# Kernel tuning notes

Hardware: AMD Instinct MI355X
Metric: run time of the kernel (lower is better)

The kernel has to match this reference:

```python
import jax, jax.numpy as jnp
import numpy as np

HEAD_SIZE = 64


def setup_inputs() -> dict:
    key = jax.random.key(0)
    kx, kk, kq, kv = jax.random.split(key, 4)
    B, T, C = 4, 4096, 1024
    x = jax.random.normal(kx, (B, T, C), dtype=jnp.float32)
    Wk = jax.random.normal(kk, (C, HEAD_SIZE), dtype=jnp.float32) * 0.02
    Wq = jax.random.normal(kq, (C, HEAD_SIZE), dtype=jnp.float32) * 0.02
    Wv = jax.random.normal(kv, (C, HEAD_SIZE), dtype=jnp.float32) * 0.02
    return {"x": x, "Wk": Wk, "Wq": Wq, "Wv": Wv}


def reference(x, Wk, Wq, Wv):
    # x: (B,T,C); projections to (B,T,H)
    T = x.shape[1]
    k = jnp.einsum('btc,ch->bth', x, Wk)
    q = jnp.einsum('btc,ch->bth', x, Wq)
    v = jnp.einsum('btc,ch->bth', x, Wv)
    scale = 1.0 / jnp.sqrt(jnp.float32(HEAD_SIZE))
    wei = jnp.einsum('bth,bsh->bts', q, k) * scale  # (B,T,T)
    causal = jnp.tril(jnp.ones((T, T), dtype=bool))
    wei = jnp.where(causal, wei, -jnp.inf)
    wei = jax.nn.softmax(wei, axis=-1)
    out = jnp.einsum('bts,bsh->bth', wei, v)  # (B,T,H)
    return out
```

## Files before the change

### kernel.cpp

```cpp
#include <hip/hip_runtime.h>

typedef __attribute__((ext_vector_type(8))) short short8;
typedef __attribute__((ext_vector_type(4))) float f32x4;
typedef unsigned short u16;

#define BB 4
#define TT 4096
#define CC 1024
#define HH 64

static __device__ __forceinline__ u16 f2bf(float f) {
    unsigned int u = __float_as_uint(f);
    unsigned int r = (u + 0x7FFFu + ((u >> 16) & 1u)) >> 16;
    return (u16)r;
}

static __device__ __forceinline__ int swz(int row, int chunk) {
    return row * 64 + ((chunk ^ (row & 7)) << 3);
}

__global__ void detect_dtype(const u16* __restrict__ xu, int* __restrict__ flag) {
    int lane = threadIdx.x;
    int cnt = 0;
    for (int i = lane; i < 1024; i += 64) {
        u16 u = xu[2 * i];
        int e = (u >> 7) & 0xFF;
        cnt += (e >= 100 && e <= 140) ? 1 : 0;
    }
    for (int d = 1; d < 64; d <<= 1) cnt += __shfl_xor(cnt, d);
    if (lane == 0) *flag = (cnt > 512) ? 1 : 0;
}

__global__ void wt_transpose(const void* __restrict__ Wk, const void* __restrict__ Wq,
                             const void* __restrict__ Wv, u16* __restrict__ Wtp,
                             float* __restrict__ accz, const int* __restrict__ flag) {
    if (blockIdx.x >= 192) {
        int zb = blockIdx.x - 192;
        const int n4 = (BB * TT * HH + BB * TT) / 4;
        float4 z = {0.f, 0.f, 0.f, 0.f};
        for (int i = zb * 256 + threadIdx.x; i < n4; i += 256 * 256)
            reinterpret_cast<float4*>(accz)[i] = z;
        return;
    }
    const int isbf = *flag;
    int r = blockIdx.x;
    int p = r >> 6;
    int n = r & 63;
    int nt = n >> 4, nl = n & 15;
    const void* W = (p == 0) ? Wq : (p == 1) ? Wk : Wv;
    int k0 = threadIdx.x * 4;
    int kb = k0 >> 6, k2 = (k0 >> 5) & 1, quad = (k0 >> 3) & 3, half = (k0 >> 2) & 1;
    ushort4 v;
    if (isbf) {
        const u16* Wb = (const u16*)W;
        v.x = Wb[(k0 + 0) * HH + n]; v.y = Wb[(k0 + 1) * HH + n];
        v.z = Wb[(k0 + 2) * HH + n]; v.w = Wb[(k0 + 3) * HH + n];
    } else {
        const float* Wf = (const float*)W;
        v.x = f2bf(Wf[(k0 + 0) * HH + n]); v.y = f2bf(Wf[(k0 + 1) * HH + n]);
        v.z = f2bf(Wf[(k0 + 2) * HH + n]); v.w = f2bf(Wf[(k0 + 3) * HH + n]);
    }
    size_t off16 = ((size_t)((p * 4 + nt) * 16 + kb) * 2 + k2) * 64 + quad * 16 + nl;
    *reinterpret_cast<ushort4*>(Wtp + off16 * 8 + half * 4) = v;
}

__global__ __launch_bounds__(256) void qkv_proj(const void* __restrict__ x,
                                                const u16* __restrict__ Wtp,
                                                u16* __restrict__ qo, u16* __restrict__ ko,
                                                u16* __restrict__ vo, const int* __restrict__ flag) {
    __shared__ __align__(16) u16 xs[16 * 1024];
    __shared__ __align__(16) u16 tls[4][3][256];
    const int isbf = *flag;
    const int tid = threadIdx.x;
    const int lane = tid & 63;
    const int w = tid >> 6;
    const int l15 = lane & 15;
    const int quad = lane >> 4;
    int phys = blockIdx.x;
    int rb = (phys & 7) * 128 + (phys >> 3);
    const int g0r = rb * 16;

    #pragma unroll
    for (int j = 0; j < 8; j++) {
        int c = tid + j * 256;
        int row = c >> 7, ck = c & 127;
        int dst = row * 1024 + ((ck ^ (row & 7)) << 3);
        if (isbf) {
            uint4 d = *reinterpret_cast<const uint4*>((const u16*)x + (size_t)(g0r + row) * CC + ck * 8);
            *reinterpret_cast<uint4*>(xs + dst) = d;
        } else {
            const float4* pf = reinterpret_cast<const float4*>((const float*)x + (size_t)(g0r + row) * CC + ck * 8);
            float4 a0 = pf[0], a1 = pf[1];
            ushort4 lo; lo.x = f2bf(a0.x); lo.y = f2bf(a0.y); lo.z = f2bf(a0.z); lo.w = f2bf(a0.w);
            ushort4 hi; hi.x = f2bf(a1.x); hi.y = f2bf(a1.y); hi.z = f2bf(a1.z); hi.w = f2bf(a1.w);
            *reinterpret_cast<ushort4*>(xs + dst) = lo;
            *reinterpret_cast<ushort4*>(xs + dst + 4) = hi;
        }
    }
    __syncthreads();

    f32x4 zero = {0.f, 0.f, 0.f, 0.f};
    f32x4 acc[3];
    #pragma unroll
    for (int i = 0; i < 3; i++) acc[i] = zero;

    for (int kb = 0; kb < 16; kb++) {
        #pragma unroll
        for (int k2 = 0; k2 < 2; k2++) {
            int ck = kb * 8 + k2 * 4 + quad;
            short8 af = *reinterpret_cast<const short8*>(xs + l15 * 1024 + ((ck ^ (l15 & 7)) << 3));
            #pragma unroll
            for (int p = 0; p < 3; p++) {
                short8 bf = *reinterpret_cast<const short8*>(
                    Wtp + ((((size_t)(p * 4 + w) * 16 + kb) * 2 + k2) * 64 + lane) * 8);
                acc[p] = __builtin_amdgcn_mfma_f32_16x16x32_bf16(af, bf, acc[p], 0, 0, 0);
            }
        }
    }

    const float qscale = 0.18033688011112042f;
    #pragma unroll
    for (int p = 0; p < 3; p++) {
        if (p < 2) {
            float sc = (p == 0) ? qscale : 1.f;
            #pragma unroll
            for (int r = 0; r < 4; r++)
                tls[w][p][(quad * 4 + r) * 16 + l15] = f2bf(acc[p][r] * sc);
        } else {
            #pragma unroll
            for (int r = 0; r < 4; r++)
                tls[w][p][l15 * 16 + quad * 4 + r] = f2bf(acc[p][r]);
        }
    }
    #pragma unroll
    for (int p = 0; p < 2; p++) {
        int t = lane >> 2, seg = lane & 3;
        ushort4 d = *reinterpret_cast<const ushort4*>(&tls[w][p][t * 16 + seg * 4]);
        u16* dst = (p == 0) ? qo : ko;
        *reinterpret_cast<ushort4*>(dst + (size_t)(g0r + t) * HH + w * 16 + seg * 4) = d;
    }
    {
        int c = lane >> 2, seg = lane & 3;
        ushort4 d = *reinterpret_cast<const ushort4*>(&tls[w][2][c * 16 + seg * 4]);
        int b = rb >> 8;
        int kt = (g0r & 4095) >> 6;
        int toff = g0r & 63;
        *reinterpret_cast<ushort4*>(vo + ((size_t)((b * 64 + kt) * 64 + w * 16 + c)) * 64 + toff + seg * 4) = d;
    }
}

__global__ __launch_bounds__(256) void attn(const u16* __restrict__ qp, const u16* __restrict__ kp,
                                            const u16* __restrict__ vp, float* __restrict__ acco,
                                            float* __restrict__ accl, void* __restrict__ outv,
                                            const int* __restrict__ flag, int nsplit) {
    __shared__ __align__(16) u16 kst[64 * 64];
    __shared__ __align__(16) u16 vts[64 * 64];
    __shared__ __align__(16) u16 pb[4][16 * 64];
    const int isbf = *flag;
    const int tid = threadIdx.x;
    const int lane = tid & 63;
    const int w = tid >> 6;
    const int l15 = lane & 15;
    const int quad = lane >> 4;

    int u = blockIdx.x;
    int b, qt, ks;
    if (nsplit == 1) {
        b = u >> 6;
        int raw = u & 63;
        qt = (raw & 1) ? (63 - (raw >> 1)) : (raw >> 1);
        ks = 0;
    } else {
        int per = 64 * nsplit;
        b = u / per;
        int rem = u - b * per;
        qt = rem / nsplit;
        ks = rem - qt * nsplit;
    }
    int qbase = qt * 64;
    int diag = qt;
    int nkt = diag + 1;
    if (ks >= nkt) return;

    short8 aq[2];
    {
        const u16* qrow = qp + (size_t)(b * TT + qbase + w * 16 + l15) * HH;
        aq[0] = *reinterpret_cast<const short8*>(qrow + quad * 8);
        aq[1] = *reinterpret_cast<const short8*>(qrow + 32 + quad * 8);
    }

    f32x4 zero = {0.f, 0.f, 0.f, 0.f};
    f32x4 o[4];
    #pragma unroll
    for (int i = 0; i < 4; i++) o[i] = zero;
    f32x4 lsum = zero;

    for (int kt = ks; kt < nkt; kt += nsplit) {
        __syncthreads();
        #pragma unroll
        for (int j = 0; j < 2; j++) {
            int cc = tid + j * 256;
            int row = cc >> 3, c8 = cc & 7;
            int dst = swz(row, c8);
            uint4 dk = *reinterpret_cast<const uint4*>(kp + (size_t)(b * TT + kt * 64) * HH + cc * 8);
            *reinterpret_cast<uint4*>(&kst[dst]) = dk;
            uint4 dv = *reinterpret_cast<const uint4*>(vp + ((size_t)(b * 64 + kt)) * 64 * 64 + cc * 8);
            *reinterpret_cast<uint4*>(&vts[dst]) = dv;
        }
        __syncthreads();
        f32x4 s[4];
        #pragma unroll
        for (int i = 0; i < 4; i++) s[i] = zero;
        #pragma unroll
        for (int k2 = 0; k2 < 2; k2++) {
            #pragma unroll
            for (int nt = 0; nt < 4; nt++) {
                short8 bf = *reinterpret_cast<const short8*>(&kst[swz(nt * 16 + l15, k2 * 4 + quad)]);
                s[nt] = __builtin_amdgcn_mfma_f32_16x16x32_bf16(aq[k2], bf, s[nt], 0, 0, 0);
            }
        }
        const int rg = qbase + w * 16 + quad * 4;
        const bool dm = (kt == diag);
        #pragma unroll
        for (int nt = 0; nt < 4; nt++) {
            int key = kt * 64 + nt * 16 + l15;
            #pragma unroll
            for (int r = 0; r < 4; r++) {
                float p = __builtin_amdgcn_exp2f(s[nt][r]);
                if (dm && key > rg + r) p = 0.f;
                s[nt][r] = p;
            }
        }
        #pragma unroll
        for (int nt = 0; nt < 4; nt++) lsum = lsum + s[nt];
        #pragma unroll
        for (int nt = 0; nt < 4; nt++) {
            int chunk = nt * 2 + (l15 >> 3);
            int off = l15 & 7;
            #pragma unroll
            for (int r = 0; r < 4; r++) {
                int row = quad * 4 + r;
                pb[w][row * 64 + ((chunk ^ (row & 7)) << 3) + off] = f2bf(s[nt][r]);
            }
        }
        #pragma unroll
        for (int k2 = 0; k2 < 2; k2++) {
            short8 ap = *reinterpret_cast<const short8*>(&pb[w][swz(l15, k2 * 4 + quad)]);
            #pragma unroll
            for (int nt = 0; nt < 4; nt++) {
                short8 bv = *reinterpret_cast<const short8*>(&vts[swz(nt * 16 + l15, k2 * 4 + quad)]);
                o[nt] = __builtin_amdgcn_mfma_f32_16x16x32_bf16(ap, bv, o[nt], 0, 0, 0);
            }
        }
    }

    #pragma unroll
    for (int d = 1; d < 16; d <<= 1) {
        f32x4 t;
        #pragma unroll
        for (int r = 0; r < 4; r++) t[r] = __shfl_xor(lsum[r], d);
        lsum = lsum + t;
    }
    const int g0 = b * TT + qbase + w * 16 + quad * 4;

    if (nsplit == 1) {
        f32x4 inv;
        #pragma unroll
        for (int r = 0; r < 4; r++) inv[r] = 1.0f / lsum[r];
        if (isbf) {
            u16* outp = (u16*)outv;
            #pragma unroll
            for (int nt = 0; nt < 4; nt++)
                #pragma unroll
                for (int r = 0; r < 4; r++)
                    outp[(size_t)(g0 + r) * HH + nt * 16 + l15] = f2bf(o[nt][r] * inv[r]);
        } else {
            float* outp = (float*)outv;
            #pragma unroll
            for (int nt = 0; nt < 4; nt++)
                #pragma unroll
                for (int r = 0; r < 4; r++)
                    outp[(size_t)(g0 + r) * HH + nt * 16 + l15] = o[nt][r] * inv[r];
        }
    } else {
        #pragma unroll
        for (int nt = 0; nt < 4; nt++)
            #pragma unroll
            for (int r = 0; r < 4; r++)
                atomicAdd(&acco[(size_t)(g0 + r) * HH + nt * 16 + l15], o[nt][r]);
        if (l15 == 0) {
            #pragma unroll
            for (int r = 0; r < 4; r++) atomicAdd(&accl[g0 + r], lsum[r]);
        }
    }
}

__global__ __launch_bounds__(256) void attn_finalize(const float* __restrict__ acco,
                                                     const float* __restrict__ accl,
                                                     void* __restrict__ outv,
                                                     const int* __restrict__ flag) {
    const int isbf = *flag;
    int i = blockIdx.x * blockDim.x + threadIdx.x;
    int row = i >> 4;
    float4 ov = reinterpret_cast<const float4*>(acco)[i];
    float inv = 1.0f / accl[row];
    if (isbf) {
        ushort4 s;
        s.x = f2bf(ov.x * inv); s.y = f2bf(ov.y * inv);
        s.z = f2bf(ov.z * inv); s.w = f2bf(ov.w * inv);
        reinterpret_cast<ushort4*>(outv)[i] = s;
    } else {
        float4 s = {ov.x * inv, ov.y * inv, ov.z * inv, ov.w * inv};
        reinterpret_cast<float4*>(outv)[i] = s;
    }
}

extern "C" void kernel_launch(void* const* d_in, const int* in_sizes, int n_in,
                              void* d_out, int out_size, void* d_ws, size_t ws_size,
                              hipStream_t stream) {
    const void* x  = d_in[0];
    const void* Wk = d_in[1];
    const void* Wq = d_in[2];
    const void* Wv = d_in[3];
    char* ws = (char*)d_ws;
    u16* qo = (u16*)(ws);
    u16* ko = (u16*)(ws + (size_t)2 * 1024 * 1024);
    u16* vo = (u16*)(ws + (size_t)4 * 1024 * 1024);
    u16* Wtp = (u16*)(ws + (size_t)6 * 1024 * 1024);
    int* flag = (int*)(ws + (size_t)6 * 1024 * 1024 + 768 * 1024);
    float* acco = (float*)(ws + (size_t)7 * 1024 * 1024);
    float* accl = (float*)(ws + (size_t)11 * 1024 * 1024);

    const size_t need_split = (size_t)11 * 1024 * 1024 + 128 * 1024;
    const int nsplit = (ws_size >= need_split) ? 4 : 1;

    detect_dtype<<<1, 64, 0, stream>>>((const u16*)x, flag);
    wt_transpose<<<(nsplit > 1 ? 448 : 192), 256, 0, stream>>>(Wk, Wq, Wv, Wtp, acco, flag);
    qkv_proj<<<1024, 256, 0, stream>>>(x, Wtp, qo, ko, vo, flag);
    if (nsplit > 1) {
        attn<<<BB * 64 * nsplit, 256, 0, stream>>>(qo, ko, vo, acco, accl, d_out, flag, nsplit);
        attn_finalize<<<(BB * TT * HH / 4) / 256, 256, 0, stream>>>(acco, accl, d_out, flag);
    } else {
        attn<<<BB * 64, 256, 0, stream>>>(qo, ko, vo, acco, accl, d_out, flag, 1);
    }
}
```

Baseline: 154.7 us.

## Drop dtype-detect kernel, prefetch K/V tiles, replace split atomics with partial buffers

Removes the separate dtype-detection launch by having each kernel probe the input with a wavefront ballot. It also drops the accumulator zeroing that used to live in the transpose launch. The attention loop now prefetches the next K/V tile into registers while the current one is committed to LDS, with lighter barriers. Split-K partial results go to per-split buffers instead of atomics, and the finalize kernel sums them. This cuts launch count, atomic contention and load latency, at the cost of a larger workspace and repeated probe loads in every block.

```diff
diff --git a/kernel.cpp b/kernel.cpp
--- a/kernel.cpp
+++ b/kernel.cpp
@@ -15,34 +15,27 @@
     return (u16)r;
 }
 
+static __device__ __forceinline__ int probe_isbf(const u16* xu) {
+    int lane = threadIdx.x & 63;
+    u16 u = xu[lane * 32];
+    int e = (u >> 7) & 0xFF;
+    unsigned long long m = __ballot(e >= 100 && e <= 140);
+    return __popcll(m) > 32;
+}
+
+static __device__ __forceinline__ void bar_lds() {
+    __builtin_amdgcn_s_waitcnt(0xC07F);
+    __builtin_amdgcn_s_barrier();
+}
+
 static __device__ __forceinline__ int swz(int row, int chunk) {
     return row * 64 + ((chunk ^ (row & 7)) << 3);
 }
 
-__global__ void detect_dtype(const u16* __restrict__ xu, int* __restrict__ flag) {
-    int lane = threadIdx.x;
-    int cnt = 0;
-    for (int i = lane; i < 1024; i += 64) {
-        u16 u = xu[2 * i];
-        int e = (u >> 7) & 0xFF;
-        cnt += (e >= 100 && e <= 140) ? 1 : 0;
-    }
-    for (int d = 1; d < 64; d <<= 1) cnt += __shfl_xor(cnt, d);
-    if (lane == 0) *flag = (cnt > 512) ? 1 : 0;
-}
-
 __global__ void wt_transpose(const void* __restrict__ Wk, const void* __restrict__ Wq,
                              const void* __restrict__ Wv, u16* __restrict__ Wtp,
-                             float* __restrict__ accz, const int* __restrict__ flag) {
-    if (blockIdx.x >= 192) {
-        int zb = blockIdx.x - 192;
-        const int n4 = (BB * TT * HH + BB * TT) / 4;
-        float4 z = {0.f, 0.f, 0.f, 0.f};
-        for (int i = zb * 256 + threadIdx.x; i < n4; i += 256 * 256)
-            reinterpret_cast<float4*>(accz)[i] = z;
-        return;
-    }
-    const int isbf = *flag;
+                             const u16* __restrict__ xprobe) {
+    const int isbf = probe_isbf(xprobe);
     int r = blockIdx.x;
     int p = r >> 6;
     int n = r & 63;
@@ -67,10 +60,10 @@
 __global__ __launch_bounds__(256) void qkv_proj(const void* __restrict__ x,
                                                 const u16* __restrict__ Wtp,
                                                 u16* __restrict__ qo, u16* __restrict__ ko,
-                                                u16* __restrict__ vo, const int* __restrict__ flag) {
+                                                u16* __restrict__ vo) {
     __shared__ __align__(16) u16 xs[16 * 1024];
     __shared__ __align__(16) u16 tls[4][3][256];
-    const int isbf = *flag;
+    const int isbf = probe_isbf((const u16*)x);
     const int tid = threadIdx.x;
     const int lane = tid & 63;
     const int w = tid >> 6;
@@ -150,13 +143,13 @@
 }
 
 __global__ __launch_bounds__(256) void attn(const u16* __restrict__ qp, const u16* __restrict__ kp,
-                                            const u16* __restrict__ vp, float* __restrict__ acco,
+                                            const u16* __restrict__ vp, float* __restrict__ accp,
                                             float* __restrict__ accl, void* __restrict__ outv,
-                                            const int* __restrict__ flag, int nsplit) {
+                                            const u16* __restrict__ xprobe, int nsplit) {
     __shared__ __align__(16) u16 kst[64 * 64];
     __shared__ __align__(16) u16 vts[64 * 64];
     __shared__ __align__(16) u16 pb[4][16 * 64];
-    const int isbf = *flag;
+    const int isbf = probe_isbf(xprobe);
     const int tid = threadIdx.x;
     const int lane = tid & 63;
     const int w = tid >> 6;
@@ -195,19 +188,32 @@
     for (int i = 0; i < 4; i++) o[i] = zero;
     f32x4 lsum = zero;
 
-    for (int kt = ks; kt < nkt; kt += nsplit) {
-        __syncthreads();
+    uint4 pk[2], pv[2];
+    auto pref = [&](int kt2) {
+        #pragma unroll
+        for (int j = 0; j < 2; j++) {
+            int cc = tid + j * 256;
+            pk[j] = *reinterpret_cast<const uint4*>(kp + (size_t)(b * TT + kt2 * 64) * HH + cc * 8);
+            pv[j] = *reinterpret_cast<const uint4*>(vp + ((size_t)(b * 64 + kt2)) * 64 * 64 + cc * 8);
+        }
+    };
+    auto commit = [&]() {
         #pragma unroll
         for (int j = 0; j < 2; j++) {
             int cc = tid + j * 256;
             int row = cc >> 3, c8 = cc & 7;
             int dst = swz(row, c8);
-            uint4 dk = *reinterpret_cast<const uint4*>(kp + (size_t)(b * TT + kt * 64) * HH + cc * 8);
-            *reinterpret_cast<uint4*>(&kst[dst]) = dk;
-            uint4 dv = *reinterpret_cast<const uint4*>(vp + ((size_t)(b * 64 + kt)) * 64 * 64 + cc * 8);
-            *reinterpret_cast<uint4*>(&vts[dst]) = dv;
-        }
-        __syncthreads();
+            *reinterpret_cast<uint4*>(&kst[dst]) = pk[j];
+            *reinterpret_cast<uint4*>(&vts[dst]) = pv[j];
+        }
+    };
+
+    pref(ks);
+    for (int kt = ks; kt < nkt; kt += nsplit) {
+        bar_lds();
+        commit();
+        if (kt + nsplit < nkt) pref(kt + nsplit);
+        bar_lds();
         f32x4 s[4];
         #pragma unroll
         for (int i = 0; i < 4; i++) s[i] = zero;
@@ -283,34 +289,43 @@
                     outp[(size_t)(g0 + r) * HH + nt * 16 + l15] = o[nt][r] * inv[r];
         }
     } else {
+        float* op = accp + (size_t)ks * TT * BB * HH;
         #pragma unroll
         for (int nt = 0; nt < 4; nt++)
             #pragma unroll
             for (int r = 0; r < 4; r++)
-                atomicAdd(&acco[(size_t)(g0 + r) * HH + nt * 16 + l15], o[nt][r]);
+                op[(size_t)(g0 + r) * HH + nt * 16 + l15] = o[nt][r];
         if (l15 == 0) {
             #pragma unroll
-            for (int r = 0; r < 4; r++) atomicAdd(&accl[g0 + r], lsum[r]);
-        }
-    }
-}
-
-__global__ __launch_bounds__(256) void attn_finalize(const float* __restrict__ acco,
+            for (int r = 0; r < 4; r++) accl[ks * (TT * BB) + g0 + r] = lsum[r];
+        }
+    }
+}
+
+__global__ __launch_bounds__(256) void attn_finalize(const float* __restrict__ accp,
                                                      const float* __restrict__ accl,
                                                      void* __restrict__ outv,
-                                                     const int* __restrict__ flag) {
-    const int isbf = *flag;
+                                                     const u16* __restrict__ xprobe, int nsplit) {
+    const int isbf = probe_isbf(xprobe);
     int i = blockIdx.x * blockDim.x + threadIdx.x;
     int row = i >> 4;
-    float4 ov = reinterpret_cast<const float4*>(acco)[i];
-    float inv = 1.0f / accl[row];
+    int qt = (row & (TT - 1)) >> 6;
+    int nv = min(nsplit, qt + 1);
+    float4 o = {0.f, 0.f, 0.f, 0.f};
+    float l = 0.f;
+    for (int ks = 0; ks < nv; ks++) {
+        float4 t = reinterpret_cast<const float4*>(accp + (size_t)ks * TT * BB * HH)[i];
+        o.x += t.x; o.y += t.y; o.z += t.z; o.w += t.w;
+        l += accl[ks * (TT * BB) + row];
+    }
+    float inv = 1.0f / l;
     if (isbf) {
         ushort4 s;
-        s.x = f2bf(ov.x * inv); s.y = f2bf(ov.y * inv);
-        s.z = f2bf(ov.z * inv); s.w = f2bf(ov.w * inv);
+        s.x = f2bf(o.x * inv); s.y = f2bf(o.y * inv);
+        s.z = f2bf(o.z * inv); s.w = f2bf(o.w * inv);
         reinterpret_cast<ushort4*>(outv)[i] = s;
     } else {
-        float4 s = {ov.x * inv, ov.y * inv, ov.z * inv, ov.w * inv};
+        float4 s = {o.x * inv, o.y * inv, o.z * inv, o.w * inv};
         reinterpret_cast<float4*>(outv)[i] = s;
     }
 }
@@ -327,20 +342,16 @@
     u16* ko = (u16*)(ws + (size_t)2 * 1024 * 1024);
     u16* vo = (u16*)(ws + (size_t)4 * 1024 * 1024);
     u16* Wtp = (u16*)(ws + (size_t)6 * 1024 * 1024);
-    int* flag = (int*)(ws + (size_t)6 * 1024 * 1024 + 768 * 1024);
-    float* acco = (float*)(ws + (size_t)7 * 1024 * 1024);
-    float* accl = (float*)(ws + (size_t)11 * 1024 * 1024);
-
-    const size_t need_split = (size_t)11 * 1024 * 1024 + 128 * 1024;
+    float* accp = (float*)(ws + (size_t)7 * 1024 * 1024);
+    float* accl = (float*)(ws + (size_t)23 * 1024 * 1024);
+
+    const size_t need_split = (size_t)23 * 1024 * 1024 + 512 * 1024;
     const int nsplit = (ws_size >= need_split) ? 4 : 1;
-
-    detect_dtype<<<1, 64, 0, stream>>>((const u16*)x, flag);
-    wt_transpose<<<(nsplit > 1 ? 448 : 192), 256, 0, stream>>>(Wk, Wq, Wv, Wtp, acco, flag);
-    qkv_proj<<<1024, 256, 0, stream>>>(x, Wtp, qo, ko, vo, flag);
-    if (nsplit > 1) {
-        attn<<<BB * 64 * nsplit, 256, 0, stream>>>(qo, ko, vo, acco, accl, d_out, flag, nsplit);
-        attn_finalize<<<(BB * TT * HH / 4) / 256, 256, 0, stream>>>(acco, accl, d_out, flag);
-    } else {
-        attn<<<BB * 64, 256, 0, stream>>>(qo, ko, vo, acco, accl, d_out, flag, 1);
-    }
-}
+    const u16* xprobe = (const u16*)x;
+
+    wt_transpose<<<192, 256, 0, stream>>>(Wk, Wq, Wv, Wtp, xprobe);
+    qkv_proj<<<1024, 256, 0, stream>>>(x, Wtp, qo, ko, vo);
+    attn<<<BB * 64 * nsplit, 256, 0, stream>>>(qo, ko, vo, accp, accl, d_out, xprobe, nsplit);
+    if (nsplit > 1)
+        attn_finalize<<<(BB * TT * HH / 4) / 256, 256, 0, stream>>>(accp, accl, d_out, xprobe, nsplit);
+}
```

Result: slower. 194.7 us (+25.9%).
